# Kernel tuning notes

Measured on AMD Instinct MI355X. Metric: run time of the kernel, lower is better.

## Reference

```python
import jax, jax.numpy as jnp
import numpy as np
import math

EMB_DIM = 1024
NUM_HEADS = 16
D_H = EMB_DIM // NUM_HEADS
B, S = 2, 2048


def setup_inputs() -> dict:
    key = jax.random.key(0)
    ks = jax.random.split(key, 6)
    limit = math.sqrt(6.0 / (EMB_DIM + D_H))  # xavier_uniform per head
    x = jax.random.normal(ks[0], (B, S, EMB_DIM), dtype=jnp.float32)
    Wq = jax.random.uniform(ks[1], (NUM_HEADS, EMB_DIM, D_H), jnp.float32, -limit, limit)
    Wk = jax.random.uniform(ks[2], (NUM_HEADS, EMB_DIM, D_H), jnp.float32, -limit, limit)
    Wv = jax.random.uniform(ks[3], (NUM_HEADS, EMB_DIM, D_H), jnp.float32, -limit, limit)
    bq = jnp.zeros((NUM_HEADS, D_H), jnp.float32)
    bk = jnp.zeros((NUM_HEADS, D_H), jnp.float32)
    bv = jnp.zeros((NUM_HEADS, D_H), jnp.float32)
    limo = math.sqrt(6.0 / (EMB_DIM + EMB_DIM))
    W_O = jax.random.uniform(ks[4], (EMB_DIM, EMB_DIM), jnp.float32, -limo, limo)
    causal_mask = jnp.tril(jnp.ones((S, S), jnp.float32))
    padding_mask = jnp.zeros((B, S), jnp.bool_)  # all-False: nothing padded
    return {"x": x, "Wq": Wq, "bq": bq, "Wk": Wk, "bk": bk, "Wv": Wv,
            "bv": bv, "W_O": W_O, "causal_mask": causal_mask,
            "padding_mask": padding_mask}


def reference(x, Wq, bq, Wk, bk, Wv, bv, W_O, causal_mask, padding_mask):
    # Per-head projections, vectorized over heads: [B,S,E] x [H,E,D] -> [B,H,S,D]
    Q = jnp.einsum('bse,hed->bhsd', x, Wq) + bq[None, :, None, :]
    K = jnp.einsum('bse,hed->bhsd', x, Wk) + bk[None, :, None, :]
    V = jnp.einsum('bse,hed->bhsd', x, Wv) + bv[None, :, None, :]
    scores = jnp.einsum('bhsd,bhtd->bhst', Q, K) / math.sqrt(D_H)
    neg_inf = jnp.float32(-jnp.inf)
    scores = jnp.where(causal_mask[None, None, :, :] == 0, neg_inf, scores)
    scores = jnp.where(padding_mask[:, None, None, :], neg_inf, scores)
    attn = jax.nn.softmax(scores, axis=-1)
    out = jnp.einsum('bhst,bhtd->bhsd', attn, V)  # [B,H,S,D]
    # concat heads in order (dim=-1) -> [B,S,H*D]
    x_concat = out.transpose(0, 2, 1, 3).reshape(B, S, EMB_DIM)
    return x_concat @ W_O
```

## Files before the change

kernel.cpp:

```cpp
#include <hip/hip_runtime.h>
#include <hip/hip_bf16.h>


typedef __hip_bfloat16 bf16;
typedef __attribute__((ext_vector_type(8))) short bfrag;
typedef __attribute__((ext_vector_type(4))) float f32x4;
typedef __attribute__((ext_vector_type(16))) float f32x16;
typedef __attribute__((ext_vector_type(4))) short short4v;

#define MFMA16(a, b, c) __builtin_amdgcn_mfma_f32_16x16x32_bf16(a, b, c, 0, 0, 0)
#define MFMA32(a, b, c) __builtin_amdgcn_mfma_f32_32x32x16_bf16(a, b, c, 0, 0, 0)

__device__ __forceinline__ unsigned pkbf(float a, float b) {
  union { bf16 h[2]; unsigned u; } w;
  w.h[0] = __float2bfloat16(a);
  w.h[1] = __float2bfloat16(b);
  return w.u;
}

__global__ __launch_bounds__(256) void prep_all(const float* __restrict__ x,
                                                const float* __restrict__ Wq,
                                                const float* __restrict__ Wk,
                                                const float* __restrict__ Wv,
                                                const float* __restrict__ Wo,
                                                bf16* __restrict__ xb,
                                                bf16* __restrict__ WqkvT,
                                                bf16* __restrict__ WoT) {
  __shared__ bf16 tile[64][80];
  int id = blockIdx.x;
  int t = threadIdx.x;
  if (id < 2048) {
    int i = id * 2048 + t * 8;
    float4 a = *(const float4*)(x + i);
    float4 b = *(const float4*)(x + i + 4);
    union { bf16 h[8]; bfrag v; } tmp;
    tmp.h[0] = __float2bfloat16(a.x); tmp.h[1] = __float2bfloat16(a.y);
    tmp.h[2] = __float2bfloat16(a.z); tmp.h[3] = __float2bfloat16(a.w);
    tmp.h[4] = __float2bfloat16(b.x); tmp.h[5] = __float2bfloat16(b.y);
    tmp.h[6] = __float2bfloat16(b.z); tmp.h[7] = __float2bfloat16(b.w);
    *(bfrag*)(xb + i) = tmp.v;
    return;
  }
  int wid = id - 2048;
  const float* src;
  bf16* dst;
  int srcld, dstld, r0, c0;
  if (wid < 768) {
    int w = wid >> 8, h = (wid >> 4) & 15;
    r0 = (wid & 15) * 64; c0 = 0;
    src = ((w == 0) ? Wq : (w == 1) ? Wk : Wv) + (long)h * 1024 * 64;
    dst = WqkvT + ((long)w * 1024 + h * 64) * 1024;
    srcld = 64; dstld = 1024;
  } else {
    int j = wid - 768;
    c0 = (j & 15) * 64; r0 = (j >> 4) * 64;
    src = Wo; dst = WoT;
    srcld = 1024; dstld = 1024;
  }
  int lr = t >> 3, lc = (t & 7) << 3;
#pragma unroll
  for (int p = 0; p < 2; ++p) {
    int r = lr + p * 32;
    const float* s = src + (long)(r0 + r) * srcld + c0 + lc;
    union { bf16 h8[8]; bfrag v; } tmp;
#pragma unroll
    for (int j = 0; j < 8; ++j) tmp.h8[j] = __float2bfloat16(s[j]);
    *(bfrag*)(&tile[r][lc]) = tmp.v;
  }
  __syncthreads();
#pragma unroll
  for (int p = 0; p < 2; ++p) {
    int c = lr + p * 32;
    union { bf16 h8[8]; bfrag v; } tmp;
#pragma unroll
    for (int j = 0; j < 8; ++j) tmp.h8[j] = tile[lc + j][c];
    *(bfrag*)(dst + (long)(c0 + c) * dstld + r0 + lc) = tmp.v;
  }
}

__global__ __launch_bounds__(256) void gemm_qkv128(const bf16* __restrict__ xb,
                                                   const bf16* __restrict__ WT,
                                                   const float* __restrict__ bq,
                                                   const float* __restrict__ bk,
                                                   const float* __restrict__ bv,
                                                   bf16* __restrict__ Q,
                                                   bf16* __restrict__ K_,
                                                   bf16* __restrict__ Vt) {
  const int K = 1024;
  __shared__ bf16 As[128][72];
  __shared__ bf16 Bs[128][72];
  int id = blockIdx.x;
  int xcd = id & 7, sw = id >> 3;
  int m0 = ((xcd << 2) | (sw & 3)) * 128;
  int n0 = (sw >> 2) * 128;
  int t = threadIdx.x, wave = t >> 6, lane = t & 63, quad = lane >> 4, col = lane & 15;
  int wr = (wave >> 1) * 64, wc = (wave & 1) * 64;
  f32x4 acc[4][4] = {};

  int srow = t >> 1, scol = (t & 1) * 32;
  const bf16* Ag = xb + (long)(m0 + srow) * K + scol;
  const bf16* Bg = WT + (long)(n0 + srow) * K + scol;

  bfrag A0[4], B0[4], A1[4], B1[4];
#pragma unroll
  for (int i = 0; i < 4; ++i) {
    A0[i] = *(const bfrag*)(Ag + 8 * i);
    B0[i] = *(const bfrag*)(Bg + 8 * i);
    A1[i] = *(const bfrag*)(Ag + 64 + 8 * i);
    B1[i] = *(const bfrag*)(Bg + 64 + 8 * i);
  }

  for (int k0 = 0; k0 < K; k0 += 64) {
    __syncthreads();
#pragma unroll
    for (int i = 0; i < 4; ++i) {
      *(bfrag*)(&As[srow][scol + 8 * i]) = A0[i];
      *(bfrag*)(&Bs[srow][scol + 8 * i]) = B0[i];
    }
    int kn = (k0 + 128 < K) ? k0 + 128 : K - 64;
#pragma unroll
    for (int i = 0; i < 4; ++i) {
      A0[i] = A1[i]; B0[i] = B1[i];
      A1[i] = *(const bfrag*)(Ag + kn + 8 * i);
      B1[i] = *(const bfrag*)(Bg + kn + 8 * i);
    }
    __syncthreads();
#pragma unroll
    for (int kc = 0; kc < 2; ++kc) {
      bfrag ra[4], rb[4];
#pragma unroll
      for (int i = 0; i < 4; ++i)
        ra[i] = *(const bfrag*)(&As[wr + 16 * i + col][kc * 32 + quad * 8]);
#pragma unroll
      for (int c = 0; c < 4; ++c)
        rb[c] = *(const bfrag*)(&Bs[wc + 16 * c + col][kc * 32 + quad * 8]);
#pragma unroll
      for (int c = 0; c < 4; ++c)
#pragma unroll
        for (int i = 0; i < 4; ++i) acc[c][i] = MFMA16(ra[i], rb[c], acc[c][i]);
    }
  }

  int sel = n0 >> 10;
  const float* bias = (sel == 0) ? bq : (sel == 1) ? bk : bv;
#pragma unroll
  for (int c = 0; c < 4; ++c) {
    int nn = (n0 + wc + 16 * c + col) & 1023;
    float bvv = bias[nn];
    int h = nn >> 6, d = nn & 63;
#pragma unroll
    for (int i = 0; i < 4; ++i) {
      int mb = m0 + wr + 16 * i + quad * 4;
      int b = mb >> 11, s0 = mb & 2047;
      if (sel < 2) {
        bf16* dst = (sel == 0) ? Q : K_;
        long base = ((long)((b << 4) + h) * 2048 + s0) * 64 + d;
#pragma unroll
        for (int r = 0; r < 4; ++r)
          dst[base + (long)r * 64] = __float2bfloat16(acc[c][i][r] + bvv);
      } else {
        union { bf16 h4[4]; short4v v; } pk;
#pragma unroll
        for (int r = 0; r < 4; ++r) pk.h4[r] = __float2bfloat16(acc[c][i][r] + bvv);
        *(short4v*)(Vt + (long)(((b << 4) + h) * 64 + d) * 2048 + s0) = pk.v;
      }
    }
  }
}

__global__ __launch_bounds__(256) void gemm_out(const bf16* __restrict__ O,
                                                const bf16* __restrict__ Bt,
                                                float* __restrict__ Cf) {
  const int K = 1024;
  __shared__ bf16 As[128][72];
  __shared__ bf16 Bs[64][72];
  int id = blockIdx.x;
  int xcd = id & 7, sw = id >> 3;
  int m0 = ((xcd << 2) | (sw & 3)) * 128;
  int n0 = (sw >> 2) * 64;
  int t = threadIdx.x;
  int wave = t >> 6, lane = t & 63, quad = lane >> 4, col = lane & 15;
  int wr = (wave >> 1) * 64, wc = (wave & 1) * 32;
  f32x4 acc[2][4] = {};

  int srA = t >> 1, scA = (t & 1) * 32;
  int srB = t >> 2, scB = (t & 3) * 16;
  int mrow = m0 + srA;
  int ob = mrow >> 11, os = mrow & 2047;
  const bf16* Ag = O + (long)ob * 2097152 + (long)os * 64 + scA;
  const bf16* Bg = Bt + (long)(n0 + srB) * K + scB;

  bfrag A0[4], A1[4];
  bfrag B0[2], B1[2];
#pragma unroll
  for (int i = 0; i < 4; ++i) {
    A0[i] = *(const bfrag*)(Ag + 8 * i);
    A1[i] = *(const bfrag*)(Ag + (long)64 * 2048 + 8 * i);
  }
#pragma unroll
  for (int i = 0; i < 2; ++i) {
    B0[i] = *(const bfrag*)(Bg + 8 * i);
    B1[i] = *(const bfrag*)(Bg + 64 + 8 * i);
  }

  for (int k0 = 0; k0 < K; k0 += 64) {
    __syncthreads();
#pragma unroll
    for (int i = 0; i < 4; ++i) *(bfrag*)(&As[srA][scA + 8 * i]) = A0[i];
#pragma unroll
    for (int i = 0; i < 2; ++i) *(bfrag*)(&Bs[srB][scB + 8 * i]) = B0[i];
    int kn = (k0 + 128 < K) ? k0 + 128 : K - 64;
#pragma unroll
    for (int i = 0; i < 4; ++i) {
      A0[i] = A1[i];
      A1[i] = *(const bfrag*)(Ag + (long)kn * 2048 + 8 * i);
    }
#pragma unroll
    for (int i = 0; i < 2; ++i) {
      B0[i] = B1[i];
      B1[i] = *(const bfrag*)(Bg + kn + 8 * i);
    }
    __syncthreads();
#pragma unroll
    for (int kc = 0; kc < 2; ++kc) {
      bfrag ra[4], rb[2];
#pragma unroll
      for (int i = 0; i < 4; ++i)
        ra[i] = *(const bfrag*)(&As[wr + 16 * i + col][kc * 32 + quad * 8]);
#pragma unroll
      for (int c = 0; c < 2; ++c)
        rb[c] = *(const bfrag*)(&Bs[wc + 16 * c + col][kc * 32 + quad * 8]);
#pragma unroll
      for (int c = 0; c < 2; ++c)
#pragma unroll
        for (int i = 0; i < 4; ++i) acc[c][i] = MFMA16(ra[i], rb[c], acc[c][i]);
    }
  }

#pragma unroll
  for (int c = 0; c < 2; ++c) {
    int n = n0 + wc + 16 * c + col;
#pragma unroll
    for (int i = 0; i < 4; ++i)
#pragma unroll
      for (int r = 0; r < 4; ++r) {
        int m = m0 + wr + 16 * i + quad * 4 + r;
        Cf[(long)m * 1024 + n] = acc[c][i][r];
      }
  }
}

__global__ __launch_bounds__(256) void attn_kernel(const bf16* __restrict__ Q,
                                                   const bf16* __restrict__ K_,
                                                   const bf16* __restrict__ Vt,
                                                   bf16* __restrict__ O) {
  int id = blockIdx.x;
  int xcd = id & 7, jj = id >> 3;
  int qt = 31 - (jj >> 2);
  int bh = ((jj & 3) << 3) | xcd;

  __shared__ bf16 Ks[128][72];
  __shared__ bf16 Vs[64][136];

  int t = threadIdx.x, wave = t >> 6, lane = t & 63;
  int qh = wave >> 1, jh = wave & 1, hi = lane >> 5, l5 = lane & 31;

  const float SC2 = 0.18033688f;

  int krow = t >> 3, kg = (t & 7) * 8;
  int vrow = t >> 4, vg = (t & 15) * 8;
  const bf16* Kbase = K_ + ((long)bh * 2048 + krow) * 64 + kg;
  const bf16* Vbase = Vt + ((long)bh * 64 + vrow) * 2048 + vg;

  int q0 = qt * 64;
  int nj = (qt >> 1) + 1;
  int qi = q0 + 32 * qh + l5;

  bfrag qa[4];
  const bf16* qp = Q + ((long)bh * 2048 + q0 + 32 * qh + l5) * 64 + hi * 8;
#pragma unroll
  for (int kd = 0; kd < 4; ++kd) qa[kd] = *(const bfrag*)(qp + kd * 16);

  f32x16 o0, o1;
  float lsum = 0.f;
#pragma unroll
  for (int r = 0; r < 16; ++r) { o0[r] = 0.f; o1[r] = 0.f; }

  bfrag kreg[4], vreg[4];
#pragma unroll
  for (int i = 0; i < 4; ++i) {
    kreg[i] = *(const bfrag*)(Kbase + (long)(32 * i) * 64);
    vreg[i] = *(const bfrag*)(Vbase + (long)(16 * i) * 2048);
  }

  for (int jt = 0; jt < nj; ++jt) {
    int j0 = jt * 128;
    __syncthreads();
#pragma unroll
    for (int i = 0; i < 4; ++i) {
      *(bfrag*)(&Ks[krow + 32 * i][kg]) = kreg[i];
      *(bfrag*)(&Vs[vrow + 16 * i][vg]) = vreg[i];
    }
    int jn = (jt + 1 < nj) ? (jt + 1) * 128 : jt * 128;
#pragma unroll
    for (int i = 0; i < 4; ++i) {
      kreg[i] = *(const bfrag*)(Kbase + (long)(jn + 32 * i) * 64);
      vreg[i] = *(const bfrag*)(Vbase + (long)(16 * i) * 2048 + jn);
    }
    __syncthreads();

    f32x16 s0, s1;
#pragma unroll
    for (int r = 0; r < 16; ++r) { s0[r] = 0.f; s1[r] = 0.f; }
    __builtin_amdgcn_s_setprio(1);
#pragma unroll
    for (int kd = 0; kd < 4; ++kd) {
      bfrag ka0 = *(const bfrag*)(&Ks[jh * 64 + l5][kd * 16 + hi * 8]);
      bfrag ka1 = *(const bfrag*)(&Ks[jh * 64 + 32 + l5][kd * 16 + hi * 8]);
      s0 = MFMA32(ka0, qa[kd], s0);
      s1 = MFMA32(ka1, qa[kd], s1);
    }
    __builtin_amdgcn_s_setprio(0);

    bool lastT = (jt == nj - 1);
    unsigned g[2][4][2];
#pragma unroll
    for (int jb = 0; jb < 2; ++jb) {
      float pv[16];
#pragma unroll
      for (int r = 0; r < 16; ++r) {
        int jl = (r & 3) + 8 * (r >> 2) + 4 * hi;
        int j = j0 + jh * 64 + jb * 32 + jl;
        float sv = jb ? s1[r] : s0[r];
        float p = __builtin_amdgcn_exp2f(fmaf(sv, SC2, -16.0f));
        if (lastT) p = (j <= qi) ? p : 0.f;
        lsum += p;
        pv[r] = p;
      }
#pragma unroll
      for (int gg = 0; gg < 4; ++gg) {
        g[jb][gg][0] = pkbf(pv[4 * gg], pv[4 * gg + 1]);
        g[jb][gg][1] = pkbf(pv[4 * gg + 2], pv[4 * gg + 3]);
      }
    }

    __builtin_amdgcn_s_setprio(1);
#pragma unroll
    for (int jb = 0; jb < 2; ++jb) {
#pragma unroll
      for (int c = 0; c < 2; ++c) {
        unsigned a0 = g[jb][2 * c][0], a1 = g[jb][2 * c][1];
        unsigned b0 = g[jb][2 * c + 1][0], b1 = g[jb][2 * c + 1][1];
        unsigned sa0 = __shfl_xor((int)a0, 32, 64);
        unsigned sa1 = __shfl_xor((int)a1, 32, 64);
        unsigned sb0 = __shfl_xor((int)b0, 32, 64);
        unsigned sb1 = __shfl_xor((int)b1, 32, 64);
        union { unsigned u[4]; bfrag f; } pf;
        pf.u[0] = hi ? sb0 : a0;
        pf.u[1] = hi ? sb1 : a1;
        pf.u[2] = hi ? b0 : sa0;
        pf.u[3] = hi ? b1 : sa1;
        int kk = jh * 64 + jb * 32 + c * 16 + hi * 8;
        bfrag av0 = *(const bfrag*)(&Vs[l5][kk]);
        bfrag av1 = *(const bfrag*)(&Vs[32 + l5][kk]);
        o0 = MFMA32(av0, pf.f, o0);
        o1 = MFMA32(av1, pf.f, o1);
      }
    }
    __builtin_amdgcn_s_setprio(0);
  }

  lsum += __shfl_xor(lsum, 32, 64);

  __syncthreads();
  float* Osc = (float*)&Ks[0][0];
  float* Lsc = (float*)&Vs[0][0];
  bf16* Of = (bf16*)((char*)&Vs[0][0] + 512);
  int q = 32 * qh + l5;
  if (jh == 1) {
#pragma unroll
    for (int r = 0; r < 16; ++r) {
      int d = (r & 3) + 8 * (r >> 2) + 4 * hi;
      Osc[q * 68 + d] = o0[r];
      Osc[q * 68 + 32 + d] = o1[r];
    }
    if (hi == 0) Lsc[q] = lsum;
  }
  __syncthreads();
  if (jh == 0) {
    float inv = 1.f / (lsum + Lsc[q]);
#pragma unroll
    for (int r = 0; r < 16; ++r) {
      int d = (r & 3) + 8 * (r >> 2) + 4 * hi;
      Of[q * 72 + d] = __float2bfloat16((o0[r] + Osc[q * 68 + d]) * inv);
      Of[q * 72 + 32 + d] = __float2bfloat16((o1[r] + Osc[q * 68 + 32 + d]) * inv);
    }
  }
  __syncthreads();
  int row = t >> 2, off = (t & 3) * 16;
  bf16* po = O + ((long)bh * 2048 + q0 + row) * 64 + off;
  *(bfrag*)(po) = *(const bfrag*)(&Of[row * 72 + off]);
  *(bfrag*)(po + 8) = *(const bfrag*)(&Of[row * 72 + off + 8]);
}

extern "C" void kernel_launch(void* const* d_in, const int* in_sizes, int n_in,
                              void* d_out, int out_size, void* d_ws, size_t ws_size,
                              hipStream_t stream) {
  const float* x  = (const float*)d_in[0];
  const float* Wq = (const float*)d_in[1];
  const float* bq = (const float*)d_in[2];
  const float* Wk = (const float*)d_in[3];
  const float* bk = (const float*)d_in[4];
  const float* Wv = (const float*)d_in[5];
  const float* bv = (const float*)d_in[6];
  const float* Wo = (const float*)d_in[7];
  float* out = (float*)d_out;

  bf16* ws = (bf16*)d_ws;
  const long MB1 = 1 << 20;
  bf16* WqkvT = ws + 0 * MB1;
  bf16* WoT   = ws + 3 * MB1;
  bf16* Q     = ws + 4 * MB1;
  bf16* K_    = ws + 8 * MB1;
  bf16* Vt    = ws + 12 * MB1;
  bf16* O     = ws + 16 * MB1;
  bf16* xb    = ws + 20 * MB1;

  prep_all<<<3072, 256, 0, stream>>>(x, Wq, Wk, Wv, Wo, xb, WqkvT, WoT);
  gemm_qkv128<<<768, 256, 0, stream>>>(xb, WqkvT, bq, bk, bv, Q, K_, Vt);
  attn_kernel<<<1024, 256, 0, stream>>>(Q, K_, Vt, O);
  gemm_out<<<512, 256, 0, stream>>>(O, WoT, out);
}
```

Measured before the change: 199.4 us.

## Use direct global-to-LDS loads with XOR swizzle and double buffering in GEMMs

Replaces the register-staged global loads in the QKV and output-projection GEMMs with global_load_lds direct-to-LDS transfers. The LDS tiles become unpadded, XOR-swizzled 32-wide K slices with two buffers, and each iteration drops from two barriers to one. The aim is to cut VGPR staging and LDS write instructions and to overlap the next tile's fetch with MFMA work. In exchange the K step halves from 64 to 32, which doubles the loop iterations and barriers, and per-stage load depth is shallower.

```diff
diff --git a/kernel.cpp b/kernel.cpp
--- a/kernel.cpp
+++ b/kernel.cpp
@@ -16,6 +16,12 @@
   w.h[0] = __float2bfloat16(a);
   w.h[1] = __float2bfloat16(b);
   return w.u;
+}
+
+__device__ __forceinline__ void gload16(const bf16* g, bf16* l) {
+  __builtin_amdgcn_global_load_lds(
+      (const __attribute__((address_space(1))) void*)(g),
+      (__attribute__((address_space(3))) void*)(l), 16, 0, 0);
 }
 
 __global__ __launch_bounds__(256) void prep_all(const float* __restrict__ x,
@@ -87,8 +93,8 @@
                                                    bf16* __restrict__ K_,
                                                    bf16* __restrict__ Vt) {
   const int K = 1024;
-  __shared__ bf16 As[128][72];
-  __shared__ bf16 Bs[128][72];
+  __shared__ bf16 As[2][128 * 32];
+  __shared__ bf16 Bs[2][128 * 32];
   int id = blockIdx.x;
   int xcd = id & 7, sw = id >> 3;
   int m0 = ((xcd << 2) | (sw & 3)) * 128;
@@ -97,49 +103,39 @@
   int wr = (wave >> 1) * 64, wc = (wave & 1) * 64;
   f32x4 acc[4][4] = {};
 
-  int srow = t >> 1, scol = (t & 1) * 32;
-  const bf16* Ag = xb + (long)(m0 + srow) * K + scol;
-  const bf16* Bg = WT + (long)(n0 + srow) * K + scol;
-
-  bfrag A0[4], B0[4], A1[4], B1[4];
-#pragma unroll
-  for (int i = 0; i < 4; ++i) {
-    A0[i] = *(const bfrag*)(Ag + 8 * i);
-    B0[i] = *(const bfrag*)(Bg + 8 * i);
-    A1[i] = *(const bfrag*)(Ag + 64 + 8 * i);
-    B1[i] = *(const bfrag*)(Bg + 64 + 8 * i);
-  }
-
-  for (int k0 = 0; k0 < K; k0 += 64) {
+  int schunk = (lane & 3) ^ ((lane >> 2) & 3);
+  const bf16* Asrc = xb + (long)(m0 + wave * 32 + (lane >> 2)) * K + schunk * 8;
+  const bf16* Bsrc = WT + (long)(n0 + wave * 32 + (lane >> 2)) * K + schunk * 8;
+  int l0 = (wave * 32) * 32;
+  int rdoff = ((quad ^ (col & 3)) << 3);
+
+#define QKV_STAGE(bi, koff)                                    \
+  {                                                            \
+    gload16(Asrc + (koff), &As[bi][l0]);                       \
+    gload16(Asrc + (koff) + 16 * K, &As[bi][l0 + 16 * 32]);    \
+    gload16(Bsrc + (koff), &Bs[bi][l0]);                       \
+    gload16(Bsrc + (koff) + 16 * K, &Bs[bi][l0 + 16 * 32]);    \
+  }
+
+  QKV_STAGE(0, 0);
+  __syncthreads();
+  for (int k0 = 0; k0 < K; k0 += 32) {
+    int cur = (k0 >> 5) & 1;
+    if (k0 + 32 < K) QKV_STAGE(cur ^ 1, k0 + 32);
+    bfrag ra[4], rb[4];
+#pragma unroll
+    for (int i = 0; i < 4; ++i)
+      ra[i] = *(const bfrag*)(&As[cur][(wr + 16 * i + col) * 32 + rdoff]);
+#pragma unroll
+    for (int c = 0; c < 4; ++c)
+      rb[c] = *(const bfrag*)(&Bs[cur][(wc + 16 * c + col) * 32 + rdoff]);
+#pragma unroll
+    for (int c = 0; c < 4; ++c)
+#pragma unroll
+      for (int i = 0; i < 4; ++i) acc[c][i] = MFMA16(ra[i], rb[c], acc[c][i]);
     __syncthreads();
-#pragma unroll
-    for (int i = 0; i < 4; ++i) {
-      *(bfrag*)(&As[srow][scol + 8 * i]) = A0[i];
-      *(bfrag*)(&Bs[srow][scol + 8 * i]) = B0[i];
-    }
-    int kn = (k0 + 128 < K) ? k0 + 128 : K - 64;
-#pragma unroll
-    for (int i = 0; i < 4; ++i) {
-      A0[i] = A1[i]; B0[i] = B1[i];
-      A1[i] = *(const bfrag*)(Ag + kn + 8 * i);
-      B1[i] = *(const bfrag*)(Bg + kn + 8 * i);
-    }
-    __syncthreads();
-#pragma unroll
-    for (int kc = 0; kc < 2; ++kc) {
-      bfrag ra[4], rb[4];
-#pragma unroll
-      for (int i = 0; i < 4; ++i)
-        ra[i] = *(const bfrag*)(&As[wr + 16 * i + col][kc * 32 + quad * 8]);
-#pragma unroll
-      for (int c = 0; c < 4; ++c)
-        rb[c] = *(const bfrag*)(&Bs[wc + 16 * c + col][kc * 32 + quad * 8]);
-#pragma unroll
-      for (int c = 0; c < 4; ++c)
-#pragma unroll
-        for (int i = 0; i < 4; ++i) acc[c][i] = MFMA16(ra[i], rb[c], acc[c][i]);
-    }
-  }
+  }
+#undef QKV_STAGE
 
   int sel = n0 >> 10;
   const float* bias = (sel == 0) ? bq : (sel == 1) ? bk : bv;
@@ -172,8 +168,8 @@
                                                 const bf16* __restrict__ Bt,
                                                 float* __restrict__ Cf) {
   const int K = 1024;
-  __shared__ bf16 As[128][72];
-  __shared__ bf16 Bs[64][72];
+  __shared__ bf16 As[2][128 * 32];
+  __shared__ bf16 Bs[2][64 * 32];
   int id = blockIdx.x;
   int xcd = id & 7, sw = id >> 3;
   int m0 = ((xcd << 2) | (sw & 3)) * 128;
@@ -183,59 +179,42 @@
   int wr = (wave >> 1) * 64, wc = (wave & 1) * 32;
   f32x4 acc[2][4] = {};
 
-  int srA = t >> 1, scA = (t & 1) * 32;
-  int srB = t >> 2, scB = (t & 3) * 16;
-  int mrow = m0 + srA;
-  int ob = mrow >> 11, os = mrow & 2047;
-  const bf16* Ag = O + (long)ob * 2097152 + (long)os * 64 + scA;
-  const bf16* Bg = Bt + (long)(n0 + srB) * K + scB;
-
-  bfrag A0[4], A1[4];
-  bfrag B0[2], B1[2];
-#pragma unroll
-  for (int i = 0; i < 4; ++i) {
-    A0[i] = *(const bfrag*)(Ag + 8 * i);
-    A1[i] = *(const bfrag*)(Ag + (long)64 * 2048 + 8 * i);
-  }
-#pragma unroll
-  for (int i = 0; i < 2; ++i) {
-    B0[i] = *(const bfrag*)(Bg + 8 * i);
-    B1[i] = *(const bfrag*)(Bg + 64 + 8 * i);
-  }
-
-  for (int k0 = 0; k0 < K; k0 += 64) {
+  int schunk = (lane & 3) ^ ((lane >> 2) & 3);
+  int arow = m0 + wave * 32 + (lane >> 2);
+  int ob = arow >> 11, os = arow & 2047;
+  const bf16* Asrc = O + (long)ob * 2097152 + (long)os * 64 + schunk * 8;
+  const bf16* Bsrc = Bt + (long)(n0 + wave * 16 + (lane >> 2)) * K + schunk * 8;
+  int la0 = (wave * 32) * 32;
+  int lb0 = (wave * 16) * 32;
+  int rdoff = ((quad ^ (col & 3)) << 3);
+
+#define OUT_STAGE(bi, k0n)                                            \
+  {                                                                   \
+    long ka = ((long)((k0n) >> 6)) * 131072 + ((k0n) & 32);           \
+    gload16(Asrc + ka, &As[bi][la0]);                                 \
+    gload16(Asrc + ka + 16 * 64, &As[bi][la0 + 16 * 32]);             \
+    gload16(Bsrc + (k0n), &Bs[bi][lb0]);                              \
+  }
+
+  OUT_STAGE(0, 0);
+  __syncthreads();
+  for (int k0 = 0; k0 < K; k0 += 32) {
+    int cur = (k0 >> 5) & 1;
+    if (k0 + 32 < K) OUT_STAGE(cur ^ 1, k0 + 32);
+    bfrag ra[4], rb[2];
+#pragma unroll
+    for (int i = 0; i < 4; ++i)
+      ra[i] = *(const bfrag*)(&As[cur][(wr + 16 * i + col) * 32 + rdoff]);
+#pragma unroll
+    for (int c = 0; c < 2; ++c)
+      rb[c] = *(const bfrag*)(&Bs[cur][(wc + 16 * c + col) * 32 + rdoff]);
+#pragma unroll
+    for (int c = 0; c < 2; ++c)
+#pragma unroll
+      for (int i = 0; i < 4; ++i) acc[c][i] = MFMA16(ra[i], rb[c], acc[c][i]);
     __syncthreads();
-#pragma unroll
-    for (int i = 0; i < 4; ++i) *(bfrag*)(&As[srA][scA + 8 * i]) = A0[i];
-#pragma unroll
-    for (int i = 0; i < 2; ++i) *(bfrag*)(&Bs[srB][scB + 8 * i]) = B0[i];
-    int kn = (k0 + 128 < K) ? k0 + 128 : K - 64;
-#pragma unroll
-    for (int i = 0; i < 4; ++i) {
-      A0[i] = A1[i];
-      A1[i] = *(const bfrag*)(Ag + (long)kn * 2048 + 8 * i);
-    }
-#pragma unroll
-    for (int i = 0; i < 2; ++i) {
-      B0[i] = B1[i];
-      B1[i] = *(const bfrag*)(Bg + kn + 8 * i);
-    }
-    __syncthreads();
-#pragma unroll
-    for (int kc = 0; kc < 2; ++kc) {
-      bfrag ra[4], rb[2];
-#pragma unroll
-      for (int i = 0; i < 4; ++i)
-        ra[i] = *(const bfrag*)(&As[wr + 16 * i + col][kc * 32 + quad * 8]);
-#pragma unroll
-      for (int c = 0; c < 2; ++c)
-        rb[c] = *(const bfrag*)(&Bs[wc + 16 * c + col][kc * 32 + quad * 8]);
-#pragma unroll
-      for (int c = 0; c < 2; ++c)
-#pragma unroll
-        for (int i = 0; i < 4; ++i) acc[c][i] = MFMA16(ra[i], rb[c], acc[c][i]);
-    }
-  }
+  }
+#undef OUT_STAGE
 
 #pragma unroll
   for (int c = 0; c < 2; ++c) {
```

After: 193.2 us. -3.1%, faster.
